# Performance work log

Hardware: AMD Instinct MI355X
Metric: run time of the kernel (lower is better)

## Reference

```python
import jax, jax.numpy as jnp
import numpy as np

EPS = 0.05  # mesh.epsilon boundary band


def _pool_one(adj, image, vs, edges):
    # adj: [N,N] bool, image: [N,F] f32, vs: [N,2] f32 in [0,1], edges: [2,E] int32
    N, F = image.shape
    E = edges.shape[1]
    K = N // 2                      # out_target
    tgt_kills = N - K               # number of vertices removed
    v0, v1 = edges[0], edges[1]
    # heap key = sum of squares of concat(image[v0], image[v1])
    cost = jnp.sum(image[v0] * image[v0], -1) + jnp.sum(image[v1] * image[v1], -1)
    def bnd(p):
        return (p[:, 0] < EPS) | (p[:, 0] > 1 - EPS) | (p[:, 1] < EPS) | (p[:, 1] > 1 - EPS)
    ok = ~(bnd(vs[v0]) | bnd(vs[v1]))   # boundary_mask = ~is_boundary
    # heappop of [value, id] lists == stable sort by cost (ties broken by edge id)
    order = jnp.argsort(cost)
    # sequential greedy collapse: kill v1 if edge interior and both endpoints alive
    def step(carry, eid):
        mask, nk = carry
        a, b = v0[eid], v1[eid]
        acc = ok[eid] & mask[a] & mask[b] & (nk < tgt_kills)
        mask = mask.at[b].set(mask[b] & ~acc)
        return (mask, nk + acc.astype(jnp.int32)), acc
    (mask, _), accepts = jax.lax.scan(step, (jnp.ones(N, bool), jnp.int32(0)), order)
    sv0, sv1 = v0[order], v1[order]
    # mapping m: dead vertex -> absorbing vertex (identity elsewhere)
    dead = jnp.where(accepts, sv1, N)          # N = out-of-range -> dropped
    m = jnp.arange(N).at[dead].set(sv0, mode='drop')
    # update_matrix: scatter-add collapsed vertex features into absorber rows
    upd = jnp.zeros_like(image).at[jnp.where(accepts, sv0, N)].add(image[sv1], mode='drop')
    image2 = image + upd
    # merge_vertex on adjacency: union rows then columns of merged vertices
    A = adj.astype(jnp.uint8)
    A1 = jnp.zeros_like(A).at[m].max(A)        # merge rows
    A2 = jnp.zeros_like(A1).at[m].max(A1.T).T  # merge cols
    alive = jnp.nonzero(mask, size=K, fill_value=0)[0]  # exactly K survivors
    adj_out = A2[alive][:, alive].astype(bool) & ~jnp.eye(K, dtype=bool)
    return adj_out, image2[alive]


def setup_inputs() -> dict:
    key = jax.random.key(0)
    k1, k2, k3, k4, k5 = jax.random.split(key, 5)
    B, N, F, E = 4, 8192, 64, 65536
    adj = jax.random.bernoulli(k1, 0.002, (B, N, N))
    image = jax.random.normal(k2, (B, N, F), jnp.float32)
    vs = jax.random.uniform(k3, (B, N, 2), dtype=jnp.float32)
    a = jax.random.randint(k4, (B, 1, E), 0, N)
    off = jax.random.randint(k5, (B, 1, E), 1, N)
    b = (a + off) % N                           # guarantee v0 != v1
    edges = jnp.concatenate([a, b], axis=1).astype(jnp.int32)
    return {"adj": adj, "image": image, "vs": vs, "edges": edges}


def reference(adj, image, vs, edges):
    # returns (pooled adjacency [B,N//2,N//2] bool, pooled features [B,N//2,F])
    return jax.vmap(_pool_one)(adj, image, vs, edges)
```

## Files before the change

### kernel.cpp

```cpp
#include <hip/hip_runtime.h>
#include <stdint.h>

typedef unsigned long long u64;
typedef unsigned int u32;
typedef unsigned char u8;

#define Bn 4
#define Nv 8192
#define Fd 64
#define Ed 65536
#define Kv 4096
#define TGTK 4096
#define NW 256
#define SC 8192

#define WS_FLAGS   ((size_t)0)
#define WS_ACCCNT  ((size_t)256)
#define WS_OUTBITS ((size_t)512)
#define OUTBITS_BYTES ((size_t)Bn*Kv*128*4)
#define WS_ZERO_BYTES (WS_OUTBITS + OUTBITS_BYTES)
#define WS_KEYS    (WS_ZERO_BYTES)
#define WS_SQ      (WS_KEYS + (size_t)Bn*Ed*8)
#define WS_BND     (WS_SQ + (size_t)Bn*Nv*4)
#define WS_MAP     (WS_BND + (size_t)Bn*Nv)
#define WS_POS     (WS_MAP + (size_t)Bn*Nv*4)
#define WS_PM      (WS_POS + (size_t)Bn*Nv*4)
#define WS_ALIVEW  (WS_PM + (size_t)Bn*Nv*4)
#define WS_ALIST   (WS_ALIVEW + (size_t)Bn*NW*4)
#define WS_ACC     (WS_ALIST + (size_t)Bn*Kv*4)
#define WS_PACK    (WS_ACC + (size_t)Bn*TGTK*2*4)
#define WS_SPACK   (WS_PACK + (size_t)Bn*Ed*4)

__global__ void k_detect(const u8* adj, u32* flags) {
    int tid = blockIdx.x * blockDim.x + threadIdx.x;
    const u32* w = (const u32*)adj;
    bool f0 = false, f1 = false, f2 = false, f3 = false;
    for (int i = tid; i < (1 << 19); i += gridDim.x * blockDim.x) {
        u32 v = w[i];
        f0 |= (v & 0x000000FFu) != 0;
        f1 |= (v & 0x0000FF00u) != 0;
        f2 |= (v & 0x00FF0000u) != 0;
        f3 |= (v & 0xFF000000u) != 0;
    }
    u32 m = 0;
    if (__ballot(f0)) m |= 1;
    if (__ballot(f1)) m |= 2;
    if (__ballot(f2)) m |= 4;
    if (__ballot(f3)) m |= 8;
    if ((threadIdx.x & 63) == 0 && m) atomicOr(flags, m);
}

__global__ void k_vertex(const float* image, const float* vs, float* sq, u8* bnd, int* map) {
#pragma clang fp contract(off)
    int idx = blockIdx.x * 256 + threadIdx.x;
    if (idx >= Bn * Nv) return;
    const float* row = image + (size_t)idx * Fd;
    float r[8];
#pragma unroll
    for (int j = 0; j < 8; ++j) r[j] = row[j] * row[j];
#pragma unroll
    for (int i = 8; i < 64; i += 8)
#pragma unroll
        for (int j = 0; j < 8; ++j) r[j] += row[i + j] * row[i + j];
    float s = ((r[0] + r[1]) + (r[2] + r[3])) + ((r[4] + r[5]) + (r[6] + r[7]));
    sq[idx] = s;
    float x = vs[(size_t)idx * 2], y = vs[(size_t)idx * 2 + 1];
    const float LO = 0.05f;
    const float HI = (float)(1.0 - 0.05);
    bnd[idx] = ((x < LO) || (x > HI) || (y < LO) || (y > HI)) ? 1 : 0;
    map[idx] = idx & (Nv - 1);
}

__global__ void k_edge(const int* edges, const float* sq, const u8* bnd, u64* keys, u32* pack) {
    int idx = blockIdx.x * 256 + threadIdx.x;
    if (idx >= Bn * Ed) return;
    int b = idx >> 16, e = idx & (Ed - 1);
    int v0 = edges[(size_t)b * 2 * Ed + e];
    int v1 = edges[(size_t)b * 2 * Ed + Ed + e];
    float c = sq[b * Nv + v0] + sq[b * Nv + v1];
    keys[idx] = ((u64)__float_as_uint(c) << 16) | (u32)e;
    u32 okk = (!bnd[b * Nv + v0] && !bnd[b * Nv + v1]) ? 1u : 0u;
    pack[idx] = (u32)v0 | ((u32)v1 << 13) | (okk << 26);
}

__device__ __forceinline__ void bitonic_cas(u64* s, int i, int pa, bool asc) {
    u64 a = s[i], c = s[pa];
    if ((a > c) == asc) { s[i] = c; s[pa] = a; }
}
__device__ __forceinline__ void cex(u64& a, u64& b, bool asc) {
    if ((a > b) == asc) { u64 t = a; a = b; b = t; }
}

__global__ __launch_bounds__(1024) void k_sortA(u64* keys) {
    __shared__ u64 s[SC];
    int b = blockIdx.x >> 3, ch = blockIdx.x & 7;
    u64* base = keys + (size_t)b * Ed + (size_t)ch * SC;
    int gb = ch * SC;
    int t8 = threadIdx.x * 8;
    u64 r[8];
#pragma unroll
    for (int u = 0; u < 8; ++u) r[u] = base[t8 + u];
    cex(r[0], r[1], true); cex(r[2], r[3], false); cex(r[4], r[5], true); cex(r[6], r[7], false);
    cex(r[0], r[2], true); cex(r[1], r[3], true); cex(r[4], r[6], false); cex(r[5], r[7], false);
    cex(r[0], r[1], true); cex(r[2], r[3], true); cex(r[4], r[5], false); cex(r[6], r[7], false);
    {
        bool a8 = (((gb + t8) & 8) == 0);
        cex(r[0], r[4], a8); cex(r[1], r[5], a8); cex(r[2], r[6], a8); cex(r[3], r[7], a8);
        cex(r[0], r[2], a8); cex(r[1], r[3], a8); cex(r[4], r[6], a8); cex(r[5], r[7], a8);
        cex(r[0], r[1], a8); cex(r[2], r[3], a8); cex(r[4], r[5], a8); cex(r[6], r[7], a8);
    }
#pragma unroll
    for (int u = 0; u < 8; ++u) s[t8 + u] = r[u];
    __syncthreads();
    for (int k = 16; k <= SC; k <<= 1) {
        for (int j = k >> 1; j >= 8; j >>= 1) {
#pragma unroll
            for (int p = 0; p < SC / 2048; ++p) {
                int t = p * 1024 + threadIdx.x;
                int i = ((t & ~(j - 1)) << 1) | (t & (j - 1));
                bool asc = (((gb + i) & k) == 0);
                bitonic_cas(s, i, i | j, asc);
            }
            __syncthreads();
        }
        bool asc = (((gb + t8) & k) == 0);
#pragma unroll
        for (int u = 0; u < 8; ++u) r[u] = s[t8 + u];
        cex(r[0], r[4], asc); cex(r[1], r[5], asc); cex(r[2], r[6], asc); cex(r[3], r[7], asc);
        cex(r[0], r[2], asc); cex(r[1], r[3], asc); cex(r[4], r[6], asc); cex(r[5], r[7], asc);
        cex(r[0], r[1], asc); cex(r[2], r[3], asc); cex(r[4], r[5], asc); cex(r[6], r[7], asc);
        if (k == SC) {
#pragma unroll
            for (int u = 0; u < 8; ++u) base[t8 + u] = r[u];
        } else {
#pragma unroll
            for (int u = 0; u < 8; ++u) s[t8 + u] = r[u];
            __syncthreads();
        }
    }
}

__global__ void k_sortB(u64* keys, int k, int j) {
    int idx = blockIdx.x * 256 + threadIdx.x;
    if (idx >= Bn * Ed / 2) return;
    int b = idx >> 15, t = idx & (Ed / 2 - 1);
    int i = ((t & ~(j - 1)) << 1) | (t & (j - 1));
    int pa = i | j;
    bool asc = ((i & k) == 0);
    u64* base = keys + (size_t)b * Ed;
    u64 a = base[i], c = base[pa];
    if ((a > c) == asc) { base[i] = c; base[pa] = a; }
}

__global__ __launch_bounds__(1024) void k_sortC(u64* keys, int k) {
    __shared__ u64 s[SC];
    int b = blockIdx.x >> 3, ch = blockIdx.x & 7;
    u64* base = keys + (size_t)b * Ed + (size_t)ch * SC;
    int gb = ch * SC;
    for (int p = 0; p < SC / 1024; ++p) s[p * 1024 + threadIdx.x] = base[p * 1024 + threadIdx.x];
    __syncthreads();
    bool asc = ((gb & k) == 0);
    for (int j = SC / 2; j >= 8; j >>= 1) {
#pragma unroll
        for (int p = 0; p < SC / 2048; ++p) {
            int t = p * 1024 + threadIdx.x;
            int i = ((t & ~(j - 1)) << 1) | (t & (j - 1));
            bitonic_cas(s, i, i | j, asc);
        }
        __syncthreads();
    }
    int t8 = threadIdx.x * 8;
    u64 r[8];
#pragma unroll
    for (int u = 0; u < 8; ++u) r[u] = s[t8 + u];
    cex(r[0], r[4], asc); cex(r[1], r[5], asc); cex(r[2], r[6], asc); cex(r[3], r[7], asc);
    cex(r[0], r[2], asc); cex(r[1], r[3], asc); cex(r[4], r[6], asc); cex(r[5], r[7], asc);
    cex(r[0], r[1], asc); cex(r[2], r[3], asc); cex(r[4], r[5], asc); cex(r[6], r[7], asc);
#pragma unroll
    for (int u = 0; u < 8; ++u) base[t8 + u] = r[u];
}

__global__ void k_gather(const u64* keys, const u32* pack, u32* spack) {
    int idx = blockIdx.x * 256 + threadIdx.x;
    if (idx >= Bn * Ed) return;
    int b = idx >> 16;
    u32 id = (u32)(keys[idx] & 0xFFFFu);
    spack[idx] = pack[(size_t)b * Ed + id];
}

__global__ __launch_bounds__(64) void k_greedy(const u32* spack, int* map, u32* aliveW,
                                               int* accList, u32* accCnt) {
    int b = blockIdx.x;
    int lane = threadIdx.x;
    __shared__ u32 alive[NW];
    __shared__ u32 mlane[Nv];
    for (int i = lane; i < NW; i += 64) alive[i] = 0xFFFFFFFFu;
    for (int i = lane; i < Nv; i += 64) mlane[i] = 64u;
    const u32* sp = spack + (size_t)b * Ed;
    u32 pc = sp[lane];
    __syncthreads();
    int nk = 0;
    const int G = Ed / 64;
    for (int g = 0; g < G; ++g) {
        u32 pn = (g + 1 < G) ? sp[(g + 1) * 64 + lane] : 0u;
        int v0 = pc & 8191;
        int v1 = (pc >> 13) & 8191;
        bool okk = (pc >> 26) & 1u;
        bool a0 = (alive[v0 >> 5] >> (v0 & 31)) & 1u;
        bool a1 = (alive[v1 >> 5] >> (v1 & 31)) & 1u;
        bool spec = okk && a0 && a1;
        if (spec) atomicMin(&mlane[v1], (u32)lane);
        __syncthreads();
        bool conf = false;
        if (spec) conf = (mlane[v0] < (u32)lane) || (mlane[v1] < (u32)lane);
        u64 specM = __ballot(spec);
        u64 confM = __ballot(conf);
        u64 accM = specM & ~confM;
        u64 rem = confM;
        while (rem) {
            int l = __ffsll((unsigned long long)rem) - 1;
            rem &= rem - 1;
            int bv0 = __shfl(v0, l);
            int bv1 = __shfl(v1, l);
            bool killer = ((accM >> lane) & 1ull) && (lane < l) && (v1 == bv0 || v1 == bv1);
            if (__ballot(killer) == 0ull) accM |= 1ull << l;
        }
        int cnt = __popcll(accM);
        int remK = TGTK - nk;
        bool acc = (accM >> lane) & 1ull;
        if (cnt > remK) {
            int rr = __popcll(accM & ((1ull << lane) - 1ull));
            if (acc && rr >= remK) acc = false;
            accM = __ballot(acc);
            cnt = remK;
        }
        if (acc) {
            atomicAnd(&alive[v1 >> 5], ~(1u << (v1 & 31)));
            map[(size_t)b * Nv + v1] = v0;
            int rr = __popcll(accM & ((1ull << lane) - 1ull));
            int slot = nk + rr;
            accList[((size_t)b * TGTK + slot) * 2] = v0;
            accList[((size_t)b * TGTK + slot) * 2 + 1] = v1;
        }
        if (spec) mlane[v1] = 64u;
        nk += cnt;
        __syncthreads();
        if (nk >= TGTK) break;
        pc = pn;
    }
    for (int i = lane; i < NW; i += 64) aliveW[b * NW + i] = alive[i];
    if (lane == 0) accCnt[b] = (u32)nk;
}

__global__ __launch_bounds__(256) void k_scan(const u32* aliveW, const int* map,
                                              int* pos, int* pm, int* alist) {
    int b = blockIdx.x, tid = threadIdx.x;
    __shared__ u32 cnt[256];
    __shared__ u32 off[256];
    u32 w = aliveW[b * NW + tid];
    cnt[tid] = __popc(w);
    __syncthreads();
    if (tid == 0) { u32 s = 0; for (int i = 0; i < 256; ++i) { off[i] = s; s += cnt[i]; } }
    __syncthreads();
    u32 base = off[tid];
    int* posb = pos + (size_t)b * Nv;
    int* alb = alist + (size_t)b * Kv;
    for (int bit = 0; bit < 32; ++bit) {
        int v = tid * 32 + bit;
        int p = -1;
        if ((w >> bit) & 1u) {
            if (base < Kv) { p = (int)base; alb[base] = v; }
            base++;
        }
        posb[v] = p;
    }
    __syncthreads();
    const int* mapb = map + (size_t)b * Nv;
    int* pmb = pm + (size_t)b * Nv;
    for (int v = tid; v < Nv; v += 256) pmb[v] = posb[mapb[v]];
}

__global__ void k_fcopy(const float* image, const int* alist, float* outF) {
    int idx = blockIdx.x * 256 + threadIdx.x;
    if (idx >= Bn * Kv * 16) return;
    int b = idx >> 16, r = idx & 65535;
    int x = r >> 4, f4 = r & 15;
    int src = alist[b * Kv + x];
    const float4* s = (const float4*)(image + ((size_t)(b * Nv + src)) * Fd) + f4;
    float4* d = (float4*)(outF + ((size_t)(b * Kv + x)) * Fd) + f4;
    *d = *s;
}

__global__ __launch_bounds__(64) void k_fscat(const float* image, const int* accList,
                                              const u32* accCnt, const int* pos, float* outF) {
    int b = blockIdx.x >> 12, e = blockIdx.x & 4095;
    if (e >= (int)accCnt[b]) return;
    int v0 = accList[((size_t)b * TGTK + e) * 2];
    int v1 = accList[((size_t)b * TGTK + e) * 2 + 1];
    int x = pos[(size_t)b * Nv + v0];
    if (x < 0) return;
    int f = threadIdx.x;
    atomicAdd(outF + ((size_t)(b * Kv + x)) * Fd + f,
              image[((size_t)(b * Nv + v1)) * Fd + f]);
}

__global__ __launch_bounds__(256) void k_merge(const u8* adj, const u32* flags,
                                               const int* pm, u32* outbits) {
    int bi = blockIdx.x;
    int b = bi >> 13, i = bi & (Nv - 1);
    int t = pm[(size_t)b * Nv + i];
    if (t < 0) return;
    __shared__ u32 bits[Kv / 32];
    int tid = threadIdx.x;
    if (tid < 128) bits[tid] = 0;
    __syncthreads();
    const int* pmb = pm + (size_t)b * Nv;
    u32 fw = flags[0];
    bool bytefmt = (fw & 1) && (fw & 8);
    auto put = [&](int col) {
        int c = pmb[col];
        if (c >= 0) atomicOr(&bits[c >> 5], 1u << (c & 31));
    };
    if (bytefmt) {
        const uint4* row = (const uint4*)(adj + ((size_t)b * Nv + i) * Nv);
#pragma unroll
        for (int it = 0; it < 2; ++it) {
            uint4 v = row[it * 256 + tid];
            if (v.x | v.y | v.z | v.w) {
                int cb = (it * 256 + tid) * 16;
                u32 wv[4] = { v.x, v.y, v.z, v.w };
                for (int q = 0; q < 4; ++q) {
                    u32 u = wv[q];
                    if (!u) continue;
#pragma unroll
                    for (int kk = 0; kk < 4; ++kk)
                        if ((u >> (8 * kk)) & 0xFFu) put(cb + q * 4 + kk);
                }
            }
        }
    } else {
        const uint4* row = (const uint4*)((const u32*)adj + ((size_t)b * Nv + i) * Nv);
        for (int it = 0; it < 8; ++it) {
            uint4 v = row[it * 256 + tid];
            int cb = (it * 256 + tid) * 4;
            if (v.x) put(cb);
            if (v.y) put(cb + 1);
            if (v.z) put(cb + 2);
            if (v.w) put(cb + 3);
        }
    }
    __syncthreads();
    if (tid < 128) {
        u32 bw = bits[tid];
        if (bw) atomicOr(&outbits[((size_t)b * Kv + t) * 128 + tid], bw);
    }
}

__global__ void k_expand(const u32* outbits, float* out) {
    int idx = blockIdx.x;
    int tid = threadIdx.x;
    int b = idx >> 14, r = idx & 16383;
    int x = r >> 2, seg = r & 3;
    int c0 = seg * 1024 + tid * 4;
    u32 w = outbits[((size_t)b * Kv + x) * 128 + (c0 >> 5)];
    u32 nib = (w >> (c0 & 31)) & 0xFu;
    float4 f;
    f.x = (nib & 1) ? 1.f : 0.f;
    f.y = (nib & 2) ? 1.f : 0.f;
    f.z = (nib & 4) ? 1.f : 0.f;
    f.w = (nib & 8) ? 1.f : 0.f;
    if (x >= c0 && x < c0 + 4) ((float*)&f)[x - c0] = 0.f;
    *((float4*)(out + ((size_t)(b * Kv + x)) * Kv + c0)) = f;
}

extern "C" void kernel_launch(void* const* d_in, const int* in_sizes, int n_in,
                              void* d_out, int out_size, void* d_ws, size_t ws_size,
                              hipStream_t stream) {
    const u8* adj = (const u8*)d_in[0];
    const float* image = (const float*)d_in[1];
    const float* vs = (const float*)d_in[2];
    const int* edges = (const int*)d_in[3];
    char* ws = (char*)d_ws;
    u32* flags = (u32*)(ws + WS_FLAGS);
    u32* accCnt = (u32*)(ws + WS_ACCCNT);
    u32* outbits = (u32*)(ws + WS_OUTBITS);
    u64* keys = (u64*)(ws + WS_KEYS);
    float* sq = (float*)(ws + WS_SQ);
    u8* bnd = (u8*)(ws + WS_BND);
    int* map = (int*)(ws + WS_MAP);
    int* pos = (int*)(ws + WS_POS);
    int* pm = (int*)(ws + WS_PM);
    u32* aliveW = (u32*)(ws + WS_ALIVEW);
    int* alist = (int*)(ws + WS_ALIST);
    int* accList = (int*)(ws + WS_ACC);
    u32* pack = (u32*)(ws + WS_PACK);
    u32* spack = (u32*)(ws + WS_SPACK);
    float* outA = (float*)d_out;
    float* outF = outA + (size_t)Bn * Kv * Kv;

    hipMemsetAsync(d_ws, 0, WS_ZERO_BYTES, stream);
    k_detect<<<64, 256, 0, stream>>>(adj, flags);
    k_vertex<<<Bn * Nv / 256, 256, 0, stream>>>(image, vs, sq, bnd, map);
    k_edge<<<Bn * Ed / 256, 256, 0, stream>>>(edges, sq, bnd, keys, pack);
    k_sortA<<<Bn * 8, 1024, 0, stream>>>(keys);
    k_sortB<<<Bn * Ed / 2 / 256, 256, 0, stream>>>(keys, 16384, 8192);
    k_sortC<<<Bn * 8, 1024, 0, stream>>>(keys, 16384);
    k_sortB<<<Bn * Ed / 2 / 256, 256, 0, stream>>>(keys, 32768, 16384);
    k_sortB<<<Bn * Ed / 2 / 256, 256, 0, stream>>>(keys, 32768, 8192);
    k_sortC<<<Bn * 8, 1024, 0, stream>>>(keys, 32768);
    k_sortB<<<Bn * Ed / 2 / 256, 256, 0, stream>>>(keys, 65536, 32768);
    k_sortB<<<Bn * Ed / 2 / 256, 256, 0, stream>>>(keys, 65536, 16384);
    k_sortB<<<Bn * Ed / 2 / 256, 256, 0, stream>>>(keys, 65536, 8192);
    k_sortC<<<Bn * 8, 1024, 0, stream>>>(keys, 65536);
    k_gather<<<Bn * Ed / 256, 256, 0, stream>>>(keys, pack, spack);
    k_greedy<<<Bn, 64, 0, stream>>>(spack, map, aliveW, accList, accCnt);
    k_scan<<<Bn, 256, 0, stream>>>(aliveW, map, pos, pm, alist);
    k_fcopy<<<Bn * Kv * 16 / 256, 256, 0, stream>>>(image, alist, outF);
    k_fscat<<<Bn * TGTK, 64, 0, stream>>>(image, accList, accCnt, pos, outF);
    k_merge<<<Bn * Nv, 256, 0, stream>>>(adj, flags, pm, outbits);
    k_expand<<<Bn * Kv * 4, 256, 0, stream>>>(outbits, outA);
}
```

Baseline: 2.013 ms.

## Sort only lowest-cost edge prefix via histogram cut, with full-sort fallback

Replaces the full 64K-edge bitonic sort per batch with a histogram of cost bins, a cut that selects roughly the cheapest 15K edges, compaction into a 16K buffer, and a sort of only that prefix before the greedy collapse. If the prefix overflows or the greedy pass does not reach the kill target, a flag triggers a single-block full sort and a greedy rerun. The boundary detection kernel is also folded into the vertex kernel. This cuts sort work and launch count, but adds atomics and a slow fallback path whose cost depends on the input distribution.

```diff
diff --git a/kernel.cpp b/kernel.cpp
--- a/kernel.cpp
+++ b/kernel.cpp
@@ -13,14 +13,23 @@
 #define TGTK 4096
 #define NW 256
 #define SC 8192
+#define SELCAP 16384
+#define SELM 15360
 
 #define WS_FLAGS   ((size_t)0)
 #define WS_ACCCNT  ((size_t)256)
-#define WS_OUTBITS ((size_t)512)
-#define OUTBITS_BYTES ((size_t)Bn*Kv*128*4)
-#define WS_ZERO_BYTES (WS_OUTBITS + OUTBITS_BYTES)
+#define WS_FB      ((size_t)512)
+#define WS_SELN    ((size_t)768)
+#define WS_CUT     ((size_t)1024)
+#define WS_HIST    ((size_t)4096)
+#define WS_OUTBITS ((size_t)131072)
+#define WS_ZERO_BYTES (WS_OUTBITS + (size_t)Bn*Kv*128*4)
 #define WS_KEYS    (WS_ZERO_BYTES)
-#define WS_SQ      (WS_KEYS + (size_t)Bn*Ed*8)
+#define WS_PACK    (WS_KEYS + (size_t)Bn*Ed*8)
+#define WS_SPACK   (WS_PACK + (size_t)Bn*Ed*4)
+#define WS_SELK    (WS_SPACK + (size_t)Bn*Ed*4)
+#define WS_SPSEL   (WS_SELK + (size_t)Bn*SELCAP*8)
+#define WS_SQ      (WS_SPSEL + (size_t)Bn*SELCAP*4)
 #define WS_BND     (WS_SQ + (size_t)Bn*Nv*4)
 #define WS_MAP     (WS_BND + (size_t)Bn*Nv)
 #define WS_POS     (WS_MAP + (size_t)Bn*Nv*4)
@@ -28,32 +37,11 @@
 #define WS_ALIVEW  (WS_PM + (size_t)Bn*Nv*4)
 #define WS_ALIST   (WS_ALIVEW + (size_t)Bn*NW*4)
 #define WS_ACC     (WS_ALIST + (size_t)Bn*Kv*4)
-#define WS_PACK    (WS_ACC + (size_t)Bn*TGTK*2*4)
-#define WS_SPACK   (WS_PACK + (size_t)Bn*Ed*4)
-
-__global__ void k_detect(const u8* adj, u32* flags) {
-    int tid = blockIdx.x * blockDim.x + threadIdx.x;
-    const u32* w = (const u32*)adj;
-    bool f0 = false, f1 = false, f2 = false, f3 = false;
-    for (int i = tid; i < (1 << 19); i += gridDim.x * blockDim.x) {
-        u32 v = w[i];
-        f0 |= (v & 0x000000FFu) != 0;
-        f1 |= (v & 0x0000FF00u) != 0;
-        f2 |= (v & 0x00FF0000u) != 0;
-        f3 |= (v & 0xFF000000u) != 0;
-    }
-    u32 m = 0;
-    if (__ballot(f0)) m |= 1;
-    if (__ballot(f1)) m |= 2;
-    if (__ballot(f2)) m |= 4;
-    if (__ballot(f3)) m |= 8;
-    if ((threadIdx.x & 63) == 0 && m) atomicOr(flags, m);
-}
-
-__global__ void k_vertex(const float* image, const float* vs, float* sq, u8* bnd, int* map) {
+
+__global__ void k_vertex(const u8* adj, u32* flags, const float* image, const float* vs,
+                         float* sq, u8* bnd, int* map) {
 #pragma clang fp contract(off)
     int idx = blockIdx.x * 256 + threadIdx.x;
-    if (idx >= Bn * Nv) return;
     const float* row = image + (size_t)idx * Fd;
     float r[8];
 #pragma unroll
@@ -69,6 +57,21 @@
     const float HI = (float)(1.0 - 0.05);
     bnd[idx] = ((x < LO) || (x > HI) || (y < LO) || (y > HI)) ? 1 : 0;
     map[idx] = idx & (Nv - 1);
+    const u32* w = (const u32*)adj;
+    bool f0 = false, f1 = false, f2 = false, f3 = false;
+    for (int i = idx; i < (1 << 19); i += 32768) {
+        u32 v = w[i];
+        f0 |= (v & 0x000000FFu) != 0;
+        f1 |= (v & 0x0000FF00u) != 0;
+        f2 |= (v & 0x00FF0000u) != 0;
+        f3 |= (v & 0xFF000000u) != 0;
+    }
+    u32 m = 0;
+    if (__ballot(f0)) m |= 1;
+    if (__ballot(f1)) m |= 2;
+    if (__ballot(f2)) m |= 4;
+    if (__ballot(f3)) m |= 8;
+    if ((threadIdx.x & 63) == 0 && m) atomicOr(flags, m);
 }
 
 __global__ void k_edge(const int* edges, const float* sq, const u8* bnd, u64* keys, u32* pack) {
@@ -83,6 +86,65 @@
     pack[idx] = (u32)v0 | ((u32)v1 << 13) | (okk << 26);
 }
 
+__device__ __forceinline__ int cost_bin(u64 key) {
+    u32 cb = (u32)(key >> 16);
+    int bin = (int)(cb >> 13) - 0x21000;
+    return bin < 0 ? 0 : (bin > 4095 ? 4095 : bin);
+}
+
+__global__ void k_hist(const u64* keys, u32* hist) {
+    int idx = blockIdx.x * 256 + threadIdx.x;
+    if (idx >= Bn * Ed) return;
+    int b = idx >> 16;
+    atomicAdd(&hist[b * 4096 + cost_bin(keys[idx])], 1u);
+}
+
+__global__ __launch_bounds__(1024) void k_cut(const u32* hist, u32* cutS, u32* fb) {
+    int b = blockIdx.x;
+    const u32* h = hist + b * 4096;
+    __shared__ u32 part[1024];
+    __shared__ u32 poff[1024];
+    __shared__ u32 cutbin;
+    int tid = threadIdx.x;
+    u32 h4[4];
+    u32 s = 0;
+#pragma unroll
+    for (int q = 0; q < 4; ++q) { h4[q] = h[tid * 4 + q]; s += h4[q]; }
+    part[tid] = s;
+    if (tid == 0) cutbin = 4095;
+    __syncthreads();
+    if (tid == 0) {
+        u32 run = 0;
+        for (int i = 0; i < 1024; ++i) { poff[i] = run; run += part[i]; }
+    }
+    __syncthreads();
+    u32 run = poff[tid];
+#pragma unroll
+    for (int q = 0; q < 4; ++q) {
+        run += h4[q];
+        if (run >= SELM) { atomicMin(&cutbin, (u32)(tid * 4 + q)); break; }
+    }
+    __syncthreads();
+    if (tid == (int)(cutbin >> 2)) {
+        u32 r2 = poff[tid];
+        for (int q = 0; q <= (int)(cutbin & 3); ++q) r2 += h4[q];
+        cutS[b * 2] = cutbin;
+        cutS[b * 2 + 1] = r2;
+        if (r2 > SELCAP) atomicOr(fb, 1u);
+    }
+}
+
+__global__ void k_select(const u64* keys, const u32* cutS, u32* selN, u64* selK) {
+    int idx = blockIdx.x * 256 + threadIdx.x;
+    if (idx >= Bn * Ed) return;
+    int b = idx >> 16;
+    u64 key = keys[idx];
+    if ((u32)cost_bin(key) <= cutS[b * 2]) {
+        u32 slot = atomicAdd(&selN[b], 1u);
+        if (slot < SELCAP) selK[(size_t)b * SELCAP + slot] = key;
+    }
+}
+
 __device__ __forceinline__ void bitonic_cas(u64* s, int i, int pa, bool asc) {
     u64 a = s[i], c = s[pa];
     if ((a > c) == asc) { s[i] = c; s[pa] = a; }
@@ -91,15 +153,16 @@
     if ((a > b) == asc) { u64 t = a; a = b; b = t; }
 }
 
-__global__ __launch_bounds__(1024) void k_sortA(u64* keys) {
+__global__ __launch_bounds__(1024) void k_sortL(u64* selK, const u32* cutS) {
     __shared__ u64 s[SC];
-    int b = blockIdx.x >> 3, ch = blockIdx.x & 7;
-    u64* base = keys + (size_t)b * Ed + (size_t)ch * SC;
+    int b = blockIdx.x >> 1, ch = blockIdx.x & 1;
+    u64* base = selK + (size_t)b * SELCAP + (size_t)ch * SC;
     int gb = ch * SC;
+    int S = (int)cutS[b * 2 + 1] - gb;
     int t8 = threadIdx.x * 8;
     u64 r[8];
 #pragma unroll
-    for (int u = 0; u < 8; ++u) r[u] = base[t8 + u];
+    for (int u = 0; u < 8; ++u) r[u] = (t8 + u < S) ? base[t8 + u] : ~0ull;
     cex(r[0], r[1], true); cex(r[2], r[3], false); cex(r[4], r[5], true); cex(r[6], r[7], false);
     cex(r[0], r[2], true); cex(r[1], r[3], true); cex(r[4], r[6], false); cex(r[5], r[7], false);
     cex(r[0], r[1], true); cex(r[2], r[3], true); cex(r[4], r[5], false); cex(r[6], r[7], false);
@@ -140,75 +203,71 @@
     }
 }
 
-__global__ void k_sortB(u64* keys, int k, int j) {
+__global__ __launch_bounds__(1024) void k_sortM(u64* selK) {
+    int b = blockIdx.x;
+    u64* base = selK + (size_t)b * SELCAP;
+    int tid = threadIdx.x;
+#pragma unroll
+    for (int p = 0; p < 8; ++p) {
+        int i = p * 1024 + tid;
+        u64 a = base[i], c = base[i + SC];
+        if (a > c) { base[i] = c; base[i + SC] = a; }
+    }
+    __syncthreads();
+    __shared__ u64 s[SC];
+    for (int h = 0; h < 2; ++h) {
+        u64* hb = base + h * SC;
+#pragma unroll
+        for (int p = 0; p < 8; ++p) s[p * 1024 + tid] = hb[p * 1024 + tid];
+        __syncthreads();
+        for (int j = SC / 2; j >= 8; j >>= 1) {
+#pragma unroll
+            for (int p = 0; p < SC / 2048; ++p) {
+                int t = p * 1024 + tid;
+                int i = ((t & ~(j - 1)) << 1) | (t & (j - 1));
+                bitonic_cas(s, i, i | j, true);
+            }
+            __syncthreads();
+        }
+        int t8 = tid * 8;
+        u64 r[8];
+#pragma unroll
+        for (int u = 0; u < 8; ++u) r[u] = s[t8 + u];
+        cex(r[0], r[4], true); cex(r[1], r[5], true); cex(r[2], r[6], true); cex(r[3], r[7], true);
+        cex(r[0], r[2], true); cex(r[1], r[3], true); cex(r[4], r[6], true); cex(r[5], r[7], true);
+        cex(r[0], r[1], true); cex(r[2], r[3], true); cex(r[4], r[5], true); cex(r[6], r[7], true);
+#pragma unroll
+        for (int u = 0; u < 8; ++u) hb[t8 + u] = r[u];
+        __syncthreads();
+    }
+}
+
+__global__ void k_gatherS(const u64* selK, const u32* pack, u32* spsel) {
     int idx = blockIdx.x * 256 + threadIdx.x;
-    if (idx >= Bn * Ed / 2) return;
-    int b = idx >> 15, t = idx & (Ed / 2 - 1);
-    int i = ((t & ~(j - 1)) << 1) | (t & (j - 1));
-    int pa = i | j;
-    bool asc = ((i & k) == 0);
-    u64* base = keys + (size_t)b * Ed;
-    u64 a = base[i], c = base[pa];
-    if ((a > c) == asc) { base[i] = c; base[pa] = a; }
-}
-
-__global__ __launch_bounds__(1024) void k_sortC(u64* keys, int k) {
-    __shared__ u64 s[SC];
-    int b = blockIdx.x >> 3, ch = blockIdx.x & 7;
-    u64* base = keys + (size_t)b * Ed + (size_t)ch * SC;
-    int gb = ch * SC;
-    for (int p = 0; p < SC / 1024; ++p) s[p * 1024 + threadIdx.x] = base[p * 1024 + threadIdx.x];
-    __syncthreads();
-    bool asc = ((gb & k) == 0);
-    for (int j = SC / 2; j >= 8; j >>= 1) {
-#pragma unroll
-        for (int p = 0; p < SC / 2048; ++p) {
-            int t = p * 1024 + threadIdx.x;
-            int i = ((t & ~(j - 1)) << 1) | (t & (j - 1));
-            bitonic_cas(s, i, i | j, asc);
-        }
-        __syncthreads();
-    }
-    int t8 = threadIdx.x * 8;
-    u64 r[8];
-#pragma unroll
-    for (int u = 0; u < 8; ++u) r[u] = s[t8 + u];
-    cex(r[0], r[4], asc); cex(r[1], r[5], asc); cex(r[2], r[6], asc); cex(r[3], r[7], asc);
-    cex(r[0], r[2], asc); cex(r[1], r[3], asc); cex(r[4], r[6], asc); cex(r[5], r[7], asc);
-    cex(r[0], r[1], asc); cex(r[2], r[3], asc); cex(r[4], r[5], asc); cex(r[6], r[7], asc);
-#pragma unroll
-    for (int u = 0; u < 8; ++u) base[t8 + u] = r[u];
-}
-
-__global__ void k_gather(const u64* keys, const u32* pack, u32* spack) {
-    int idx = blockIdx.x * 256 + threadIdx.x;
-    if (idx >= Bn * Ed) return;
-    int b = idx >> 16;
-    u32 id = (u32)(keys[idx] & 0xFFFFu);
-    spack[idx] = pack[(size_t)b * Ed + id];
-}
-
-__global__ __launch_bounds__(64) void k_greedy(const u32* spack, int* map, u32* aliveW,
-                                               int* accList, u32* accCnt) {
-    int b = blockIdx.x;
-    int lane = threadIdx.x;
-    __shared__ u32 alive[NW];
-    __shared__ u32 mlane[Nv];
+    if (idx >= Bn * SELCAP) return;
+    int b = idx >> 14;
+    u32 id = (u32)(selK[idx] & 0xFFFFu);
+    spsel[idx] = pack[(size_t)b * Ed + id];
+}
+
+__device__ __forceinline__ void greedy_core(const u32* sp, int S, int b, int lane,
+        u32* alive, u32* mlane, int* map, u32* aliveW, int* accList, u32* accCnt, u32* fb) {
     for (int i = lane; i < NW; i += 64) alive[i] = 0xFFFFFFFFu;
     for (int i = lane; i < Nv; i += 64) mlane[i] = 64u;
-    const u32* sp = spack + (size_t)b * Ed;
+    __syncthreads();
+    int nk = 0;
+    int G = (S + 63) >> 6;
     u32 pc = sp[lane];
-    __syncthreads();
-    int nk = 0;
-    const int G = Ed / 64;
+    bool done = false;
     for (int g = 0; g < G; ++g) {
         u32 pn = (g + 1 < G) ? sp[(g + 1) * 64 + lane] : 0u;
+        bool valid = (g * 64 + lane) < S;
         int v0 = pc & 8191;
         int v1 = (pc >> 13) & 8191;
         bool okk = (pc >> 26) & 1u;
         bool a0 = (alive[v0 >> 5] >> (v0 & 31)) & 1u;
         bool a1 = (alive[v1 >> 5] >> (v1 & 31)) & 1u;
-        bool spec = okk && a0 && a1;
+        bool spec = valid && okk && a0 && a1;
         if (spec) atomicMin(&mlane[v1], (u32)lane);
         __syncthreads();
         bool conf = false;
@@ -245,11 +304,93 @@
         if (spec) mlane[v1] = 64u;
         nk += cnt;
         __syncthreads();
-        if (nk >= TGTK) break;
+        if (nk >= TGTK) { done = true; break; }
         pc = pn;
     }
     for (int i = lane; i < NW; i += 64) aliveW[b * NW + i] = alive[i];
-    if (lane == 0) accCnt[b] = (u32)nk;
+    if (lane == 0) {
+        accCnt[b] = (u32)nk;
+        if (!done && nk < TGTK && fb) atomicOr(fb, 1u);
+    }
+}
+
+__global__ __launch_bounds__(64) void k_greedyP(const u32* spsel, const u32* cutS, int* map,
+        u32* aliveW, int* accList, u32* accCnt, u32* fb) {
+    __shared__ u32 alive[NW];
+    __shared__ u32 mlane[Nv];
+    int b = blockIdx.x;
+    int S = (int)cutS[b * 2 + 1];
+    if (S > SELCAP) S = SELCAP;
+    greedy_core(spsel + (size_t)b * SELCAP, S, b, threadIdx.x, alive, mlane,
+                map, aliveW, accList, accCnt, fb);
+}
+
+__global__ __launch_bounds__(1024) void k_sortFB(u64* keys, const u32* pack, u32* spackF,
+                                                 const u32* fb) {
+    if (*fb == 0) return;
+    int b = blockIdx.x;
+    u64* kb = keys + (size_t)b * Ed;
+    __shared__ u64 s[SC];
+    int tid = threadIdx.x;
+    for (int ch = 0; ch < 8; ++ch) {
+        u64* cb = kb + ch * SC;
+        int gb = ch * SC;
+        for (int p = 0; p < 8; ++p) s[p * 1024 + tid] = cb[p * 1024 + tid];
+        __syncthreads();
+        for (int k = 2; k <= SC; k <<= 1)
+            for (int j = k >> 1; j > 0; j >>= 1) {
+                for (int p = 0; p < 4; ++p) {
+                    int t = p * 1024 + tid;
+                    int i = ((t & ~(j - 1)) << 1) | (t & (j - 1));
+                    bool asc = (((gb + i) & k) == 0);
+                    bitonic_cas(s, i, i | j, asc);
+                }
+                __syncthreads();
+            }
+        for (int p = 0; p < 8; ++p) cb[p * 1024 + tid] = s[p * 1024 + tid];
+        __syncthreads();
+    }
+    for (int k = 16384; k <= 65536; k <<= 1) {
+        for (int j = k >> 1; j >= SC; j >>= 1) {
+            for (int p = 0; p < 32; ++p) {
+                int t = p * 1024 + tid;
+                int i = ((t & ~(j - 1)) << 1) | (t & (j - 1));
+                bool asc = ((i & k) == 0);
+                u64 a = kb[i], c = kb[i | j];
+                if ((a > c) == asc) { kb[i] = c; kb[i | j] = a; }
+            }
+            __syncthreads();
+        }
+        for (int ch = 0; ch < 8; ++ch) {
+            u64* cb = kb + ch * SC;
+            bool asc = (((ch * SC) & k) == 0);
+            for (int p = 0; p < 8; ++p) s[p * 1024 + tid] = cb[p * 1024 + tid];
+            __syncthreads();
+            for (int j = SC / 2; j > 0; j >>= 1) {
+                for (int p = 0; p < 4; ++p) {
+                    int t = p * 1024 + tid;
+                    int i = ((t & ~(j - 1)) << 1) | (t & (j - 1));
+                    bitonic_cas(s, i, i | j, asc);
+                }
+                __syncthreads();
+            }
+            for (int p = 0; p < 8; ++p) cb[p * 1024 + tid] = s[p * 1024 + tid];
+            __syncthreads();
+        }
+    }
+    for (int i = tid; i < Ed; i += 1024)
+        spackF[(size_t)b * Ed + i] = pack[(size_t)b * Ed + (u32)(kb[i] & 0xFFFFu)];
+}
+
+__global__ __launch_bounds__(64) void k_greedyF(const u32* spackF, int* map, u32* aliveW,
+        int* accList, u32* accCnt, const u32* fb) {
+    if (*fb == 0) return;
+    __shared__ u32 alive[NW];
+    __shared__ u32 mlane[Nv];
+    int b = blockIdx.x;
+    for (int i = threadIdx.x; i < Nv; i += 64) map[(size_t)b * Nv + i] = i;
+    greedy_core(spackF + (size_t)b * Ed, Ed, b, threadIdx.x, alive, mlane,
+                map, aliveW, accList, accCnt, nullptr);
 }
 
 __global__ __launch_bounds__(256) void k_scan(const u32* aliveW, const int* map,
@@ -383,8 +524,16 @@
     char* ws = (char*)d_ws;
     u32* flags = (u32*)(ws + WS_FLAGS);
     u32* accCnt = (u32*)(ws + WS_ACCCNT);
+    u32* fb = (u32*)(ws + WS_FB);
+    u32* selN = (u32*)(ws + WS_SELN);
+    u32* cutS = (u32*)(ws + WS_CUT);
+    u32* hist = (u32*)(ws + WS_HIST);
     u32* outbits = (u32*)(ws + WS_OUTBITS);
     u64* keys = (u64*)(ws + WS_KEYS);
+    u32* pack = (u32*)(ws + WS_PACK);
+    u32* spackF = (u32*)(ws + WS_SPACK);
+    u64* selK = (u64*)(ws + WS_SELK);
+    u32* spsel = (u32*)(ws + WS_SPSEL);
     float* sq = (float*)(ws + WS_SQ);
     u8* bnd = (u8*)(ws + WS_BND);
     int* map = (int*)(ws + WS_MAP);
@@ -393,27 +542,21 @@
     u32* aliveW = (u32*)(ws + WS_ALIVEW);
     int* alist = (int*)(ws + WS_ALIST);
     int* accList = (int*)(ws + WS_ACC);
-    u32* pack = (u32*)(ws + WS_PACK);
-    u32* spack = (u32*)(ws + WS_SPACK);
     float* outA = (float*)d_out;
     float* outF = outA + (size_t)Bn * Kv * Kv;
 
     hipMemsetAsync(d_ws, 0, WS_ZERO_BYTES, stream);
-    k_detect<<<64, 256, 0, stream>>>(adj, flags);
-    k_vertex<<<Bn * Nv / 256, 256, 0, stream>>>(image, vs, sq, bnd, map);
+    k_vertex<<<Bn * Nv / 256, 256, 0, stream>>>(adj, flags, image, vs, sq, bnd, map);
     k_edge<<<Bn * Ed / 256, 256, 0, stream>>>(edges, sq, bnd, keys, pack);
-    k_sortA<<<Bn * 8, 1024, 0, stream>>>(keys);
-    k_sortB<<<Bn * Ed / 2 / 256, 256, 0, stream>>>(keys, 16384, 8192);
-    k_sortC<<<Bn * 8, 1024, 0, stream>>>(keys, 16384);
-    k_sortB<<<Bn * Ed / 2 / 256, 256, 0, stream>>>(keys, 32768, 16384);
-    k_sortB<<<Bn * Ed / 2 / 256, 256, 0, stream>>>(keys, 32768, 8192);
-    k_sortC<<<Bn * 8, 1024, 0, stream>>>(keys, 32768);
-    k_sortB<<<Bn * Ed / 2 / 256, 256, 0, stream>>>(keys, 65536, 32768);
-    k_sortB<<<Bn * Ed / 2 / 256, 256, 0, stream>>>(keys, 65536, 16384);
-    k_sortB<<<Bn * Ed / 2 / 256, 256, 0, stream>>>(keys, 65536, 8192);
-    k_sortC<<<Bn * 8, 1024, 0, stream>>>(keys, 65536);
-    k_gather<<<Bn * Ed / 256, 256, 0, stream>>>(keys, pack, spack);
-    k_greedy<<<Bn, 64, 0, stream>>>(spack, map, aliveW, accList, accCnt);
+    k_hist<<<Bn * Ed / 256, 256, 0, stream>>>(keys, hist);
+    k_cut<<<Bn, 1024, 0, stream>>>(hist, cutS, fb);
+    k_select<<<Bn * Ed / 256, 256, 0, stream>>>(keys, cutS, selN, selK);
+    k_sortL<<<Bn * 2, 1024, 0, stream>>>(selK, cutS);
+    k_sortM<<<Bn, 1024, 0, stream>>>(selK);
+    k_gatherS<<<Bn * SELCAP / 256, 256, 0, stream>>>(selK, pack, spsel);
+    k_greedyP<<<Bn, 64, 0, stream>>>(spsel, cutS, map, aliveW, accList, accCnt, fb);
+    k_sortFB<<<Bn, 1024, 0, stream>>>(keys, pack, spackF, fb);
+    k_greedyF<<<Bn, 64, 0, stream>>>(spackF, map, aliveW, accList, accCnt, fb);
     k_scan<<<Bn, 256, 0, stream>>>(aliveW, map, pos, pm, alist);
     k_fcopy<<<Bn * Kv * 16 / 256, 256, 0, stream>>>(image, alist, outF);
     k_fscat<<<Bn * TGTK, 64, 0, stream>>>(image, accList, accCnt, pos, outF);
```

Measured after the change: 3.823 ms. 1.9x slower.
